# Optimization experiments

Hardware: AMD Instinct MI355X
Metric: run time of the kernel (lower is better)

## Reference

```python
import jax, jax.numpy as jnp
import numpy as np

N_SRC, N_DST, N_EDGES = 60000, 50000, 600000
IN_DIM, OUT_DIM = 256, 128


def setup_inputs() -> dict:
    key = jax.random.key(0)
    k1, k2, k3, k4, k5, k6 = jax.random.split(key, 6)
    features = jax.random.normal(k1, (N_SRC, IN_DIM), dtype=jnp.float32)
    t = jax.random.uniform(k2, (N_SRC,), dtype=jnp.float32)
    edge_src = jax.random.randint(k3, (N_EDGES,), 0, N_SRC, dtype=jnp.int32)
    edge_dst = jax.random.randint(k4, (N_EDGES,), 0, N_DST, dtype=jnp.int32)
    # learned params: xavier_normal with relu gain for fc, default for temporal_fc
    gain = float(np.sqrt(2.0))
    std_fc = gain * np.sqrt(2.0 / (IN_DIM + OUT_DIM))
    W_fc = jax.random.normal(k5, (OUT_DIM, IN_DIM), dtype=jnp.float32) * std_fc
    W_t = jax.random.normal(k6, (1, OUT_DIM), dtype=jnp.float32) * (1.0 / np.sqrt(OUT_DIM))
    return {"features": features, "t": t, "edge_src": edge_src,
            "edge_dst": edge_dst, "n_dst": N_DST, "W_fc": W_fc, "W_t": W_t}


def reference(features, t, edge_src, edge_dst, n_dst, W_fc, W_t):
    # z = fc(h), no bias
    z = features @ W_fc.T                      # [n_src, out_dim]
    s = (z @ W_t.T)[:, 0]                      # temporal_fc(z) -> [n_src]
    # edge attention: e = -|t_src - t_dst| (non-differentiable in original)
    e = jax.lax.stop_gradient(-jnp.abs(t[edge_src] - t[edge_dst]))  # [E]
    # mailbox logits: exp(temporal_fc(z_src) * e / 500)
    y = jnp.exp(s[edge_src] * e / 500.0)       # [E]
    # segment softmax over incoming edges of each dst node
    m = jax.ops.segment_max(y, edge_dst, num_segments=n_dst)
    m = jnp.where(jnp.isfinite(m), m, 0.0)     # empty mailboxes
    ex = jnp.exp(y - m[edge_dst])
    denom = jax.ops.segment_sum(ex, edge_dst, num_segments=n_dst)
    alpha = ex / denom[edge_dst]               # [E]
    # weighted neighbor sum
    h = jax.ops.segment_sum(alpha[:, None] * z[edge_src], edge_dst, num_segments=n_dst)
    # residual
    return z[:n_dst] + h
```

## Files before the change

kernel.cpp:

```cpp
#include <hip/hip_runtime.h>
#include <cstdint>

#define NBINS 1024
#define EPB   4096
#define MAXE  1536

typedef __attribute__((ext_vector_type(8))) _Float16 half8;
typedef __attribute__((ext_vector_type(4))) float floatx4;

__global__ __launch_bounds__(512, 4) void gemm_hist(
    const float* __restrict__ A, const float* __restrict__ W,
    const float* __restrict__ Wt, const int* __restrict__ edst,
    _Float16* __restrict__ z16, float* __restrict__ s,
    int* __restrict__ gcount, int M, int E, int NBH)
{
    __shared__ __align__(16) unsigned char smem[65536];

    if ((int)blockIdx.x < NBH) {
        int* h = (int*)smem;
        for (int i = threadIdx.x; i < NBINS; i += 512) h[i] = 0;
        __syncthreads();
        int base = blockIdx.x * EPB + threadIdx.x * 8;
        if (base + 8 <= E) {
            int4 d0 = *(const int4*)(edst + base);
            int4 d1 = *(const int4*)(edst + base + 4);
            atomicAdd(&h[d0.x >> 6], 1); atomicAdd(&h[d0.y >> 6], 1);
            atomicAdd(&h[d0.z >> 6], 1); atomicAdd(&h[d0.w >> 6], 1);
            atomicAdd(&h[d1.x >> 6], 1); atomicAdd(&h[d1.y >> 6], 1);
            atomicAdd(&h[d1.z >> 6], 1); atomicAdd(&h[d1.w >> 6], 1);
        } else {
            for (int i = 0; i < 8; ++i)
                if (base + i < E) atomicAdd(&h[edst[base + i] >> 6], 1);
        }
        __syncthreads();
        for (int i = threadIdx.x; i < NBINS; i += 512)
            gcount[(size_t)blockIdx.x * NBINS + i] = h[i];
        return;
    }

    half8* Wlds = (half8*)smem;
    const int tile = blockIdx.x - NBH;
    const int tid  = threadIdx.x;
    const int lane = tid & 63;
    const int w    = tid >> 6;
    const int m    = lane & 15;
    const int q    = lane >> 4;

#pragma unroll
    for (int it = 0; it < 8; ++it) {
        int pair = w * 8 + it;
        int nt = pair & 7, ks = pair >> 3;
        const float* src = W + (size_t)(nt * 16 + m) * 256 + ks * 32 + q * 8;
        float4 w0 = *(const float4*)src;
        float4 w1 = *(const float4*)(src + 4);
        half8 h;
        h[0] = (_Float16)w0.x; h[1] = (_Float16)w0.y;
        h[2] = (_Float16)w0.z; h[3] = (_Float16)w0.w;
        h[4] = (_Float16)w1.x; h[5] = (_Float16)w1.y;
        h[6] = (_Float16)w1.z; h[7] = (_Float16)w1.w;
        Wlds[pair * 64 + lane] = h;
    }

    const int row_base = tile * 128 + w * 16;
    const int arow = min(row_base + m, M - 1);
    const float* ap = A + (size_t)arow * 256 + q * 8;

    float4 abuf[8];
#pragma unroll
    for (int i = 0; i < 4; ++i) {
        abuf[2 * i]     = *(const float4*)(ap + i * 32);
        abuf[2 * i + 1] = *(const float4*)(ap + i * 32 + 4);
    }

    floatx4 acc[8];
#pragma unroll
    for (int nt = 0; nt < 8; ++nt) acc[nt] = (floatx4){0.f, 0.f, 0.f, 0.f};

    __syncthreads();

#pragma unroll
    for (int ks = 0; ks < 8; ++ks) {
        float4 a0 = abuf[(ks & 3) * 2];
        float4 a1 = abuf[(ks & 3) * 2 + 1];
        half8 af;
        af[0] = (_Float16)a0.x; af[1] = (_Float16)a0.y;
        af[2] = (_Float16)a0.z; af[3] = (_Float16)a0.w;
        af[4] = (_Float16)a1.x; af[5] = (_Float16)a1.y;
        af[6] = (_Float16)a1.z; af[7] = (_Float16)a1.w;

        if (ks < 4) {
            abuf[(ks & 3) * 2]     = *(const float4*)(ap + (ks + 4) * 32);
            abuf[(ks & 3) * 2 + 1] = *(const float4*)(ap + (ks + 4) * 32 + 4);
        }

#pragma unroll
        for (int nt = 0; nt < 8; ++nt) {
            half8 bf = Wlds[(ks * 8 + nt) * 64 + lane];
            acc[nt] = __builtin_amdgcn_mfma_f32_16x16x32_f16(
                af, bf, acc[nt], 0, 0, 0);
        }
    }

    float wt[8];
#pragma unroll
    for (int nt = 0; nt < 8; ++nt) wt[nt] = Wt[nt * 16 + m];

    float sp[4] = {0.f, 0.f, 0.f, 0.f};
#pragma unroll
    for (int nt = 0; nt < 8; ++nt)
#pragma unroll
        for (int reg = 0; reg < 4; ++reg)
            sp[reg] += acc[nt][reg] * wt[nt];

#pragma unroll
    for (int reg = 0; reg < 4; ++reg) {
        int row = row_base + q * 4 + reg;
        if (row < M) {
#pragma unroll
            for (int nt = 0; nt < 8; ++nt)
                z16[(size_t)row * 128 + nt * 16 + m] = (_Float16)acc[nt][reg];
        }
    }
#pragma unroll
    for (int off = 1; off <= 8; off <<= 1)
#pragma unroll
        for (int reg = 0; reg < 4; ++reg)
            sp[reg] += __shfl_xor(sp[reg], off, 64);
    if (m == 0) {
#pragma unroll
        for (int reg = 0; reg < 4; ++reg) {
            int row = row_base + q * 4 + reg;
            if (row < M) s[row] = sp[reg];
        }
    }
}

__global__ __launch_bounds__(256) void part_scan(
    int* __restrict__ gcount, int* __restrict__ binTot, int NB)
{
    int b    = blockIdx.x * 4 + (threadIdx.x >> 6);
    int lane = threadIdx.x & 63;
    if (b >= NBINS) return;
    int chunks = (NB + 63) >> 6;
    int run = 0;
    for (int c = 0; c < chunks; ++c) {
        int blk = c * 64 + lane;
        int v = (blk < NB) ? gcount[(size_t)blk * NBINS + b] : 0;
        int incl = v;
#pragma unroll
        for (int off = 1; off < 64; off <<= 1) {
            int n = __shfl_up(incl, off, 64);
            if (lane >= off) incl += n;
        }
        if (blk < NB) gcount[(size_t)blk * NBINS + b] = run + incl - v;
        run += __shfl(incl, 63, 64);
    }
    if (lane == 0) binTot[b] = run;
}

__global__ __launch_bounds__(1024) void part_scanB(
    const int* __restrict__ binTot, int* __restrict__ binstart)
{
    __shared__ int sb[NBINS];
    int b = threadIdx.x;
    int v = binTot[b];
    sb[b] = v;
    __syncthreads();
    for (int off = 1; off < NBINS; off <<= 1) {
        int add = (b >= off) ? sb[b - off] : 0;
        __syncthreads();
        sb[b] += add;
        __syncthreads();
    }
    binstart[b] = sb[b] - v;
    if (b == NBINS - 1) binstart[NBINS] = sb[b];
}

__global__ __launch_bounds__(512) void part_scatter(
    const int* __restrict__ esrc, const int* __restrict__ edst,
    const float* __restrict__ t, const float* __restrict__ s,
    const int* __restrict__ gcount, const int* __restrict__ binstart,
    int2* __restrict__ part, int E)
{
    __shared__ int hloc[NBINS];
    __shared__ int hbase[NBINS];
    for (int i = threadIdx.x; i < NBINS; i += 512) hloc[i] = 0;
    __syncthreads();

    int base = blockIdx.x * EPB + threadIdx.x * 8;
    int si[8], di[8], rk[8];
    int nv = 0;
    if (base < E) {
        nv = E - base; if (nv > 8) nv = 8;
        if (nv == 8) {
            int4 s0 = *(const int4*)(esrc + base);
            int4 s1 = *(const int4*)(esrc + base + 4);
            int4 d0 = *(const int4*)(edst + base);
            int4 d1 = *(const int4*)(edst + base + 4);
            si[0]=s0.x; si[1]=s0.y; si[2]=s0.z; si[3]=s0.w;
            si[4]=s1.x; si[5]=s1.y; si[6]=s1.z; si[7]=s1.w;
            di[0]=d0.x; di[1]=d0.y; di[2]=d0.z; di[3]=d0.w;
            di[4]=d1.x; di[5]=d1.y; di[6]=d1.z; di[7]=d1.w;
        } else {
            for (int i = 0; i < 8; ++i) {
                int e = min(base + i, E - 1);
                si[i] = esrc[e]; di[i] = edst[e];
            }
        }
#pragma unroll
        for (int i = 0; i < 8; ++i)
            if (i < nv) rk[i] = atomicAdd(&hloc[di[i] >> 6], 1);
    }

    for (int i = threadIdx.x; i < NBINS; i += 512)
        hbase[i] = binstart[i] + gcount[(size_t)blockIdx.x * NBINS + i];
    __syncthreads();

#pragma unroll
    for (int i = 0; i < 8; ++i) {
        if (i < nv) {
            float ee = -fabsf(t[si[i]] - t[di[i]]);
            float exv = __expf(__expf(s[si[i]] * ee * (1.0f / 500.0f)));
            part[hbase[di[i] >> 6] + rk[i]] =
                make_int2((si[i] & 0xffff) | ((di[i] & 63) << 16),
                          __float_as_int(exv));
        }
    }
}

__global__ __launch_bounds__(256) void aggregate(
    const _Float16* __restrict__ z16, const int* __restrict__ binstart,
    const int2* __restrict__ part, float* __restrict__ out, int Nd)
{
    __shared__ int2 arr[MAXE];
    __shared__ int lcnt[64];
    __shared__ int loff[65];

    const int tid = threadIdx.x;
    const int b = blockIdx.x;
    const int s0 = binstart[b];
    int nE = binstart[b + 1] - s0;
    if (nE > MAXE) nE = MAXE;

    if (tid < 64) lcnt[tid] = 0;
    __syncthreads();

    int2 rec[6]; int rrk[6], rloc[6], nrec = 0;
    for (int i = tid; i < nE; i += 256) {
        int2 r = part[s0 + i];
        int loc = (r.x >> 16) & 63;
        rec[nrec] = r;
        rloc[nrec] = loc;
        rrk[nrec] = atomicAdd(&lcnt[loc], 1);
        ++nrec;
    }
    __syncthreads();
    if (tid < 64) {
        int v = lcnt[tid], x = v;
#pragma unroll
        for (int off = 1; off < 64; off <<= 1) {
            int n = __shfl_up(x, off, 64);
            if (tid >= off) x += n;
        }
        loff[tid + 1] = x;
        if (tid == 0) loff[0] = 0;
    }
    __syncthreads();
    for (int i = 0; i < nrec; ++i)
        arr[loff[rloc[i]] + rrk[i]] = rec[i];
    __syncthreads();

    const int lane = tid & 63;
    const int w = tid >> 6;
    const int g = lane >> 3;
    const int c = lane & 7;

    const int loc0 = w * 16 + g;
    const int loc1 = loc0 + 8;
    const int jb0 = loff[loc0], je0 = loff[loc0 + 1];
    const int jb1 = loff[loc1], je1 = loff[loc1 + 1];
    int j0 = jb0, j1 = jb1;

    float acc0[16], acc1[16];
#pragma unroll
    for (int i = 0; i < 16; ++i) { acc0[i] = 0.f; acc1[i] = 0.f; }
    float ds0 = 0.f, ds1 = 0.f;

    while (j0 < je0 || j1 < je1) {
        bool vA0 = j0 < je0,     vB0 = j0 + 1 < je0;
        bool vA1 = j1 < je1,     vB1 = j1 + 1 < je1;
        int2 rA0 = arr[vA0 ? j0     : 0];
        int2 rB0 = arr[vB0 ? j0 + 1 : 0];
        int2 rA1 = arr[vA1 ? j1     : 0];
        int2 rB1 = arr[vB1 ? j1 + 1 : 0];
        float xA0 = vA0 ? __int_as_float(rA0.y) : 0.f;
        float xB0 = vB0 ? __int_as_float(rB0.y) : 0.f;
        float xA1 = vA1 ? __int_as_float(rA1.y) : 0.f;
        float xB1 = vB1 ? __int_as_float(rB1.y) : 0.f;
        const half8* pA0 = (const half8*)(z16 + (size_t)(rA0.x & 0xffff) * 128 + c * 16);
        const half8* pB0 = (const half8*)(z16 + (size_t)(rB0.x & 0xffff) * 128 + c * 16);
        const half8* pA1 = (const half8*)(z16 + (size_t)(rA1.x & 0xffff) * 128 + c * 16);
        const half8* pB1 = (const half8*)(z16 + (size_t)(rB1.x & 0xffff) * 128 + c * 16);
        half8 a0lo = pA0[0], a0hi = pA0[1];
        half8 b0lo = pB0[0], b0hi = pB0[1];
        half8 a1lo = pA1[0], a1hi = pA1[1];
        half8 b1lo = pB1[0], b1hi = pB1[1];
        ds0 += xA0 + xB0;
        ds1 += xA1 + xB1;
#pragma unroll
        for (int i = 0; i < 8; ++i) {
            acc0[i]     = fmaf(xA0, (float)a0lo[i], acc0[i]);
            acc0[8 + i] = fmaf(xA0, (float)a0hi[i], acc0[8 + i]);
            acc0[i]     = fmaf(xB0, (float)b0lo[i], acc0[i]);
            acc0[8 + i] = fmaf(xB0, (float)b0hi[i], acc0[8 + i]);
            acc1[i]     = fmaf(xA1, (float)a1lo[i], acc1[i]);
            acc1[8 + i] = fmaf(xA1, (float)a1hi[i], acc1[8 + i]);
            acc1[i]     = fmaf(xB1, (float)b1lo[i], acc1[i]);
            acc1[8 + i] = fmaf(xB1, (float)b1hi[i], acc1[8 + i]);
        }
        j0 += 2; j1 += 2;
    }

#pragma unroll
    for (int half = 0; half < 2; ++half) {
        int d = b * 64 + (half ? loc1 : loc0);
        if (d >= Nd) continue;
        float ds = half ? ds1 : ds0;
        float* ac = half ? acc1 : acc0;
        bool has = half ? (je1 > jb1) : (je0 > jb0);
        float inv = has ? 1.0f / ds : 0.0f;
        const half8* zr = (const half8*)(z16 + (size_t)d * 128 + c * 16);
        half8 r0 = zr[0], r1 = zr[1];
        float* op = out + (size_t)d * 128 + c * 16;
        *(float4*)(op + 0)  = make_float4(fmaf(ac[0],  inv, (float)r0[0]),
                                          fmaf(ac[1],  inv, (float)r0[1]),
                                          fmaf(ac[2],  inv, (float)r0[2]),
                                          fmaf(ac[3],  inv, (float)r0[3]));
        *(float4*)(op + 4)  = make_float4(fmaf(ac[4],  inv, (float)r0[4]),
                                          fmaf(ac[5],  inv, (float)r0[5]),
                                          fmaf(ac[6],  inv, (float)r0[6]),
                                          fmaf(ac[7],  inv, (float)r0[7]));
        *(float4*)(op + 8)  = make_float4(fmaf(ac[8],  inv, (float)r1[0]),
                                          fmaf(ac[9],  inv, (float)r1[1]),
                                          fmaf(ac[10], inv, (float)r1[2]),
                                          fmaf(ac[11], inv, (float)r1[3]));
        *(float4*)(op + 12) = make_float4(fmaf(ac[12], inv, (float)r1[4]),
                                          fmaf(ac[13], inv, (float)r1[5]),
                                          fmaf(ac[14], inv, (float)r1[6]),
                                          fmaf(ac[15], inv, (float)r1[7]));
    }
}

extern "C" void kernel_launch(void* const* d_in, const int* in_sizes, int n_in,
                              void* d_out, int out_size, void* d_ws, size_t ws_size,
                              hipStream_t stream)
{
    const float* features = (const float*)d_in[0];
    const float* t        = (const float*)d_in[1];
    const int*   esrc     = (const int*)d_in[2];
    const int*   edst     = (const int*)d_in[3];
    const float* Wfc      = (const float*)d_in[5];
    const float* Wt       = (const float*)d_in[6];
    float* out = (float*)d_out;

    const int M  = in_sizes[1];
    const int E  = in_sizes[2];
    const int OD = in_sizes[6];
    const int Nd = out_size / OD;

    const int NBH = (E + EPB - 1) / EPB;
    const int GB  = (M + 127) / 128;

    _Float16* z16      = (_Float16*)d_ws;
    float*    s        = (float*)(z16 + (size_t)M * 128);
    int*      gcount   = (int*)(s + M);
    int*      binTot   = gcount + (size_t)NBH * NBINS;
    int*      binstart = binTot + NBINS;
    int2*     part     = (int2*)(binstart + NBINS + 4);

    gemm_hist<<<NBH + GB, 512, 0, stream>>>(features, Wfc, Wt, edst,
                                            z16, s, gcount, M, E, NBH);
    part_scan<<<NBINS / 4, 256, 0, stream>>>(gcount, binTot, NBH);
    part_scanB<<<1, 1024, 0, stream>>>(binTot, binstart);
    part_scatter<<<NBH, 512, 0, stream>>>(esrc, edst, t, s, gcount, binstart,
                                          part, E);
    aggregate<<<(Nd + 63) / 64, 256, 0, stream>>>(z16, binstart, part, out, Nd);
}
```

Before: 177.4 us.

## Fuse bin-total scan into part_scan, halve edges per block, unroll aggregation by four

The separate single-block part_scanB kernel is removed. Its work now runs in whichever part_scan block finishes last, detected with an atomic counter and thread fences, which saves one kernel launch. Edges per block for the histogram and scatter are halved to 2048, doubling block count and parallelism at the cost of a larger per-block count table to scan. The aggregate loop now processes four edges per destination per iteration instead of two, putting more gathers in flight at the cost of more registers.

```diff
diff --git a/kernel.cpp b/kernel.cpp
--- a/kernel.cpp
+++ b/kernel.cpp
@@ -2,7 +2,7 @@
 #include <cstdint>
 
 #define NBINS 1024
-#define EPB   4096
+#define EPB   2048
 #define MAXE  1536
 
 typedef __attribute__((ext_vector_type(8))) _Float16 half8;
@@ -12,24 +12,23 @@
     const float* __restrict__ A, const float* __restrict__ W,
     const float* __restrict__ Wt, const int* __restrict__ edst,
     _Float16* __restrict__ z16, float* __restrict__ s,
-    int* __restrict__ gcount, int M, int E, int NBH)
+    int* __restrict__ gcount, int* __restrict__ done,
+    int M, int E, int NBH)
 {
     __shared__ __align__(16) unsigned char smem[65536];
 
     if ((int)blockIdx.x < NBH) {
+        if (blockIdx.x == 0 && threadIdx.x == 0) *done = 0;
         int* h = (int*)smem;
         for (int i = threadIdx.x; i < NBINS; i += 512) h[i] = 0;
         __syncthreads();
-        int base = blockIdx.x * EPB + threadIdx.x * 8;
-        if (base + 8 <= E) {
+        int base = blockIdx.x * EPB + threadIdx.x * 4;
+        if (base + 4 <= E) {
             int4 d0 = *(const int4*)(edst + base);
-            int4 d1 = *(const int4*)(edst + base + 4);
             atomicAdd(&h[d0.x >> 6], 1); atomicAdd(&h[d0.y >> 6], 1);
             atomicAdd(&h[d0.z >> 6], 1); atomicAdd(&h[d0.w >> 6], 1);
-            atomicAdd(&h[d1.x >> 6], 1); atomicAdd(&h[d1.y >> 6], 1);
-            atomicAdd(&h[d1.z >> 6], 1); atomicAdd(&h[d1.w >> 6], 1);
         } else {
-            for (int i = 0; i < 8; ++i)
+            for (int i = 0; i < 4; ++i)
                 if (base + i < E) atomicAdd(&h[edst[base + i] >> 6], 1);
         }
         __syncthreads();
@@ -136,11 +135,11 @@
 }
 
 __global__ __launch_bounds__(256) void part_scan(
-    int* __restrict__ gcount, int* __restrict__ binTot, int NB)
+    int* __restrict__ gcount, int* __restrict__ binTot,
+    int* __restrict__ binstart, int* __restrict__ done, int NB)
 {
     int b    = blockIdx.x * 4 + (threadIdx.x >> 6);
     int lane = threadIdx.x & 63;
-    if (b >= NBINS) return;
     int chunks = (NB + 63) >> 6;
     int run = 0;
     for (int c = 0; c < chunks; ++c) {
@@ -156,24 +155,33 @@
         run += __shfl(incl, 63, 64);
     }
     if (lane == 0) binTot[b] = run;
-}
-
-__global__ __launch_bounds__(1024) void part_scanB(
-    const int* __restrict__ binTot, int* __restrict__ binstart)
-{
-    __shared__ int sb[NBINS];
-    int b = threadIdx.x;
-    int v = binTot[b];
-    sb[b] = v;
-    __syncthreads();
-    for (int off = 1; off < NBINS; off <<= 1) {
-        int add = (b >= off) ? sb[b - off] : 0;
+
+    __threadfence();
+    __shared__ int isLast;
+    if (threadIdx.x == 0)
+        isLast = (atomicAdd(done, 1) == (int)gridDim.x - 1) ? 1 : 0;
+    __syncthreads();
+    if (!isLast) return;
+    __threadfence();
+
+    const int tid = threadIdx.x;
+    int4 v4 = *(const int4*)(binTot + tid * 4);
+    int tsum = v4.x + v4.y + v4.z + v4.w;
+    __shared__ int sb[256];
+    sb[tid] = tsum;
+    __syncthreads();
+    for (int off = 1; off < 256; off <<= 1) {
+        int add = (tid >= off) ? sb[tid - off] : 0;
         __syncthreads();
-        sb[b] += add;
+        sb[tid] += add;
         __syncthreads();
     }
-    binstart[b] = sb[b] - v;
-    if (b == NBINS - 1) binstart[NBINS] = sb[b];
+    int excl = sb[tid] - tsum;
+    binstart[tid * 4 + 0] = excl;
+    binstart[tid * 4 + 1] = excl + v4.x;
+    binstart[tid * 4 + 2] = excl + v4.x + v4.y;
+    binstart[tid * 4 + 3] = excl + v4.x + v4.y + v4.z;
+    if (tid == 255) binstart[NBINS] = sb[255];
 }
 
 __global__ __launch_bounds__(512) void part_scatter(
@@ -187,28 +195,24 @@
     for (int i = threadIdx.x; i < NBINS; i += 512) hloc[i] = 0;
     __syncthreads();
 
-    int base = blockIdx.x * EPB + threadIdx.x * 8;
-    int si[8], di[8], rk[8];
+    int base = blockIdx.x * EPB + threadIdx.x * 4;
+    int si[4], di[4], rk[4];
     int nv = 0;
     if (base < E) {
-        nv = E - base; if (nv > 8) nv = 8;
-        if (nv == 8) {
+        nv = E - base; if (nv > 4) nv = 4;
+        if (nv == 4) {
             int4 s0 = *(const int4*)(esrc + base);
-            int4 s1 = *(const int4*)(esrc + base + 4);
             int4 d0 = *(const int4*)(edst + base);
-            int4 d1 = *(const int4*)(edst + base + 4);
             si[0]=s0.x; si[1]=s0.y; si[2]=s0.z; si[3]=s0.w;
-            si[4]=s1.x; si[5]=s1.y; si[6]=s1.z; si[7]=s1.w;
             di[0]=d0.x; di[1]=d0.y; di[2]=d0.z; di[3]=d0.w;
-            di[4]=d1.x; di[5]=d1.y; di[6]=d1.z; di[7]=d1.w;
         } else {
-            for (int i = 0; i < 8; ++i) {
+            for (int i = 0; i < 4; ++i) {
                 int e = min(base + i, E - 1);
                 si[i] = esrc[e]; di[i] = edst[e];
             }
         }
 #pragma unroll
-        for (int i = 0; i < 8; ++i)
+        for (int i = 0; i < 4; ++i)
             if (i < nv) rk[i] = atomicAdd(&hloc[di[i] >> 6], 1);
     }
 
@@ -217,7 +221,7 @@
     __syncthreads();
 
 #pragma unroll
-    for (int i = 0; i < 8; ++i) {
+    for (int i = 0; i < 4; ++i) {
         if (i < nv) {
             float ee = -fabsf(t[si[i]] - t[di[i]]);
             float exv = __expf(__expf(s[si[i]] * ee * (1.0f / 500.0f)));
@@ -287,38 +291,36 @@
     float ds0 = 0.f, ds1 = 0.f;
 
     while (j0 < je0 || j1 < je1) {
-        bool vA0 = j0 < je0,     vB0 = j0 + 1 < je0;
-        bool vA1 = j1 < je1,     vB1 = j1 + 1 < je1;
-        int2 rA0 = arr[vA0 ? j0     : 0];
-        int2 rB0 = arr[vB0 ? j0 + 1 : 0];
-        int2 rA1 = arr[vA1 ? j1     : 0];
-        int2 rB1 = arr[vB1 ? j1 + 1 : 0];
-        float xA0 = vA0 ? __int_as_float(rA0.y) : 0.f;
-        float xB0 = vB0 ? __int_as_float(rB0.y) : 0.f;
-        float xA1 = vA1 ? __int_as_float(rA1.y) : 0.f;
-        float xB1 = vB1 ? __int_as_float(rB1.y) : 0.f;
-        const half8* pA0 = (const half8*)(z16 + (size_t)(rA0.x & 0xffff) * 128 + c * 16);
-        const half8* pB0 = (const half8*)(z16 + (size_t)(rB0.x & 0xffff) * 128 + c * 16);
-        const half8* pA1 = (const half8*)(z16 + (size_t)(rA1.x & 0xffff) * 128 + c * 16);
-        const half8* pB1 = (const half8*)(z16 + (size_t)(rB1.x & 0xffff) * 128 + c * 16);
-        half8 a0lo = pA0[0], a0hi = pA0[1];
-        half8 b0lo = pB0[0], b0hi = pB0[1];
-        half8 a1lo = pA1[0], a1hi = pA1[1];
-        half8 b1lo = pB1[0], b1hi = pB1[1];
-        ds0 += xA0 + xB0;
-        ds1 += xA1 + xB1;
-#pragma unroll
-        for (int i = 0; i < 8; ++i) {
-            acc0[i]     = fmaf(xA0, (float)a0lo[i], acc0[i]);
-            acc0[8 + i] = fmaf(xA0, (float)a0hi[i], acc0[8 + i]);
-            acc0[i]     = fmaf(xB0, (float)b0lo[i], acc0[i]);
-            acc0[8 + i] = fmaf(xB0, (float)b0hi[i], acc0[8 + i]);
-            acc1[i]     = fmaf(xA1, (float)a1lo[i], acc1[i]);
-            acc1[8 + i] = fmaf(xA1, (float)a1hi[i], acc1[8 + i]);
-            acc1[i]     = fmaf(xB1, (float)b1lo[i], acc1[i]);
-            acc1[8 + i] = fmaf(xB1, (float)b1hi[i], acc1[8 + i]);
-        }
-        j0 += 2; j1 += 2;
+        int2 r[8]; float x[8];
+#pragma unroll
+        for (int k = 0; k < 4; ++k) {
+            bool v0 = (j0 + k) < je0;
+            bool v1 = (j1 + k) < je1;
+            r[k]     = arr[v0 ? j0 + k : 0];
+            r[4 + k] = arr[v1 ? j1 + k : 0];
+            x[k]     = v0 ? __int_as_float(r[k].y)     : 0.f;
+            x[4 + k] = v1 ? __int_as_float(r[4 + k].y) : 0.f;
+        }
+        half8 lo[8], hi[8];
+#pragma unroll
+        for (int k = 0; k < 8; ++k) {
+            const half8* p =
+                (const half8*)(z16 + (size_t)(r[k].x & 0xffff) * 128 + c * 16);
+            lo[k] = p[0];
+            hi[k] = p[1];
+        }
+#pragma unroll
+        for (int k = 0; k < 4; ++k) { ds0 += x[k]; ds1 += x[4 + k]; }
+#pragma unroll
+        for (int k = 0; k < 4; ++k)
+#pragma unroll
+            for (int i = 0; i < 8; ++i) {
+                acc0[i]     = fmaf(x[k],     (float)lo[k][i],     acc0[i]);
+                acc0[8 + i] = fmaf(x[k],     (float)hi[k][i],     acc0[8 + i]);
+                acc1[i]     = fmaf(x[4 + k], (float)lo[4 + k][i], acc1[i]);
+                acc1[8 + i] = fmaf(x[4 + k], (float)hi[4 + k][i], acc1[8 + i]);
+            }
+        j0 += 4; j1 += 4;
     }
 
 #pragma unroll
@@ -376,12 +378,13 @@
     int*      gcount   = (int*)(s + M);
     int*      binTot   = gcount + (size_t)NBH * NBINS;
     int*      binstart = binTot + NBINS;
-    int2*     part     = (int2*)(binstart + NBINS + 4);
+    int*      done     = binstart + NBINS + 4;
+    int2*     part     = (int2*)(done + 4);
 
     gemm_hist<<<NBH + GB, 512, 0, stream>>>(features, Wfc, Wt, edst,
-                                            z16, s, gcount, M, E, NBH);
-    part_scan<<<NBINS / 4, 256, 0, stream>>>(gcount, binTot, NBH);
-    part_scanB<<<1, 1024, 0, stream>>>(binTot, binstart);
+                                            z16, s, gcount, done, M, E, NBH);
+    part_scan<<<NBINS / 4, 256, 0, stream>>>(gcount, binTot, binstart, done,
+                                             NBH);
     part_scatter<<<NBH, 512, 0, stream>>>(esrc, edst, t, s, gcount, binstart,
                                           part, E);
     aggregate<<<(Nd + 63) / 64, 256, 0, stream>>>(z16, binstart, part, out, Nd);
```

After: 206.1 us. 1.16x slower.
